# Optimization experiments

Measured on AMD Instinct MI355X. Metric: run time of the kernel, lower is better.

Reference implementation:

```python
import jax, jax.numpy as jnp
import numpy as np

# nuScenes-scale config: batch 2, 360x360 BEV grid (1440/4), 128 channels,
# 10 classes, 200 proposals, 3x3 NMS kernel, 40k occupied voxels per sample.
B, H, W_GRID, NUM_CLS, NUM_PROP, NMS_K = 2, 360, 360, 10, 200, 3
C = 128
N_PER_B = 40000
NEG_FILL = -1000000.0  # scatter_nd fill value from to_dense()


def _bev_pos():
    # replicates create_2D_grid: coord = (x_index_along_dim1, y_index_along_dim0)
    xs = jnp.arange(H, dtype=jnp.float32)
    ys = jnp.arange(W_GRID, dtype=jnp.float32)
    by, bx = jnp.meshgrid(xs, ys, indexing='ij')  # by[i,j]=i, bx[i,j]=j
    return jnp.stack([bx, by], axis=-1).reshape(-1, 2)  # [H*W, 2]


def setup_inputs() -> dict:
    key = jax.random.key(0)
    ks = jax.random.split(key, 10)
    # unique spatial locations per batch sample (sparse voxel coords)
    flats = [jax.random.permutation(ks[i], H * W_GRID)[:N_PER_B] for i in range(B)]
    flat = jnp.concatenate(flats)
    b = jnp.repeat(jnp.arange(B), N_PER_B)
    indices = jnp.stack([b, flat // W_GRID, flat % W_GRID], axis=1).astype(jnp.int32)
    features = jax.random.normal(ks[4], (B * N_PER_B, C), jnp.float32)
    # heatmap head (pointwise linears standing in for the submconv stack)
    W_hm1 = jax.random.normal(ks[5], (C, C), jnp.float32) * (2.0 / C) ** 0.5
    b_hm1 = jnp.zeros((C,), jnp.float32)
    W_hm2 = jax.random.normal(ks[6], (C, NUM_CLS), jnp.float32) * (2.0 / C) ** 0.5
    b_hm2 = jnp.full((NUM_CLS,), -2.19, jnp.float32)  # fc[-1].bias.fill_(-2.19)
    # class_encoding: nn.Conv1d(num_class, channels, 1)
    W_cls = jax.random.normal(ks[7], (C, NUM_CLS), jnp.float32) * 0.1
    b_cls = jnp.zeros((C,), jnp.float32)
    return dict(features=features, W_hm1=W_hm1, b_hm1=b_hm1, W_hm2=W_hm2,
                b_hm2=b_hm2, W_cls=W_cls, b_cls=b_cls, indices=indices)


def reference(features, W_hm1, b_hm1, W_hm2, b_hm2, W_cls, b_cls, indices):
    bidx, yi, xi = indices[:, 0], indices[:, 1], indices[:, 2]
    HW = H * W_GRID

    # --- x.dense(): scatter voxel features to dense BEV grid (zero fill) ---
    xd = jnp.zeros((B, H, W_GRID, C), features.dtype).at[bidx, yi, xi].set(features)
    x_flat = xd.reshape(B, HW, C).transpose(0, 2, 1)  # [B, C, HW]

    # --- heatmap head (per-voxel) then to_dense() with -1e6 fill ---
    hm = jax.nn.relu(features @ W_hm1 + b_hm1) @ W_hm2 + b_hm2  # [N, NUM_CLS]
    dense_hm = jnp.full((B, H, W_GRID, NUM_CLS), NEG_FILL, hm.dtype)
    dense_hm = dense_hm.at[bidx, yi, xi].set(hm).transpose(0, 3, 1, 2)  # [B,K,H,W]

    heat = jax.nn.sigmoid(dense_hm)  # detached in original

    # --- NMS-kernel peak extraction ---
    pad = NMS_K // 2
    inner = jax.lax.reduce_window(heat, -jnp.inf, jax.lax.max,
                                  (1, 1, NMS_K, NMS_K), (1, 1, 1, 1), 'VALID')
    local_max = jnp.zeros_like(heat).at[:, :, pad:H - pad, pad:W_GRID - pad].set(inner)
    # pedestrian (8) and traffic_cone (9): kernel size 1
    local_max = local_max.at[:, 8].set(heat[:, 8]).at[:, 9].set(heat[:, 9])
    heat = heat * (heat == local_max)
    heat_f = heat.reshape(B, NUM_CLS, HW)

    # --- top-k proposals over (class, location) ---
    _, top = jax.lax.top_k(heat_f.reshape(B, -1), NUM_PROP)  # [B, P]
    cls = top // HW
    idx = top % HW

    # --- gather proposal features + class encoding ---
    qf = jnp.take_along_axis(x_flat, jnp.broadcast_to(idx[:, None, :], (B, C, NUM_PROP)), axis=2)
    onehot = jax.nn.one_hot(cls, NUM_CLS, dtype=qf.dtype)  # [B, P, K]
    qf = qf + jnp.einsum('ck,bpk->bcp', W_cls, onehot) + b_cls[None, :, None]

    # --- proposal positions and heatmap scores ---
    query_pos = _bev_pos()[idx]  # [B, P, 2]
    qhs = jnp.take_along_axis(heat_f, jnp.broadcast_to(idx[:, None, :], (B, NUM_CLS, NUM_PROP)), axis=2)
    return qf, query_pos, qhs, cls
```

## Files before the change

kernel.cpp:

```cpp
#include <hip/hip_runtime.h>

#define HW 129600
#define WG 360
#define HG 360
#define NCLS 10
#define NPROP 200
#define CDIM 128
#define NROWS 80000
#define NB 2
#define SEL_CAP 4096
#define HIST_BINS 16384
#define CHUNK 8192

__device__ __forceinline__ float nms_val(const float* __restrict__ hp, int pos,
                                         int cl) {
  float v = hp[pos];
  if (cl >= 8) return v;
  int y = pos / WG, x = pos - y * WG;
  if (y == 0 || y == HG - 1 || x == 0 || x == WG - 1) return 0.f;
  float m = v;
  m = fmaxf(m, hp[pos - 1]);
  m = fmaxf(m, hp[pos + 1]);
  m = fmaxf(m, hp[pos - WG - 1]);
  m = fmaxf(m, hp[pos - WG]);
  m = fmaxf(m, hp[pos - WG + 1]);
  m = fmaxf(m, hp[pos + WG - 1]);
  m = fmaxf(m, hp[pos + WG]);
  m = fmaxf(m, hp[pos + WG + 1]);
  return (v == m) ? v : 0.f;
}

__global__ __launch_bounds__(128) void k_head(
    const float* __restrict__ feat, const float* __restrict__ W1,
    const float* __restrict__ b1, const float* __restrict__ W2,
    const float* __restrict__ b2, const int* __restrict__ idxs,
    float* __restrict__ dense_heat, int* __restrict__ rowmap) {
  __shared__ __align__(16) float lds_w[32 * 128];
  __shared__ __align__(16) float lds_f[32 * 32];
  __shared__ __align__(16) float lds_w2t[NCLS * 128];
  __shared__ int lds_b[32];
  __shared__ int lds_p[32];
  const int tid = threadIdx.x;
  const int row0 = blockIdx.x * 32;
  const int tc = tid & 31;
  const int tr = tid >> 5;

  float acc[8][4];
#pragma unroll
  for (int r = 0; r < 8; ++r) {
#pragma unroll
    for (int c = 0; c < 4; ++c) acc[r][c] = 0.f;
  }

  for (int kt = 0; kt < 4; ++kt) {
#pragma unroll
    for (int i = 0; i < 8; ++i) {
      int fi = tid + i * 128;
      *(float4*)(lds_w + fi * 4) = *(const float4*)(W1 + kt * 4096 + fi * 4);
    }
#pragma unroll
    for (int i = 0; i < 2; ++i) {
      int fi = tid + i * 128;
      int r = fi >> 3, kq = fi & 7;
      *(float4*)(lds_f + r * 32 + kq * 4) =
          *(const float4*)(feat + (size_t)(row0 + r) * CDIM + kt * 32 + kq * 4);
    }
    __syncthreads();
#pragma unroll
    for (int kg = 0; kg < 8; ++kg) {
      float4 w0 = *(const float4*)(lds_w + (kg * 4 + 0) * 128 + tc * 4);
      float4 w1 = *(const float4*)(lds_w + (kg * 4 + 1) * 128 + tc * 4);
      float4 w2 = *(const float4*)(lds_w + (kg * 4 + 2) * 128 + tc * 4);
      float4 w3 = *(const float4*)(lds_w + (kg * 4 + 3) * 128 + tc * 4);
#pragma unroll
      for (int r = 0; r < 8; ++r) {
        float4 fv = *(const float4*)(lds_f + (tr * 8 + r) * 32 + kg * 4);
        acc[r][0] = fmaf(fv.x, w0.x, acc[r][0]);
        acc[r][0] = fmaf(fv.y, w1.x, acc[r][0]);
        acc[r][0] = fmaf(fv.z, w2.x, acc[r][0]);
        acc[r][0] = fmaf(fv.w, w3.x, acc[r][0]);
        acc[r][1] = fmaf(fv.x, w0.y, acc[r][1]);
        acc[r][1] = fmaf(fv.y, w1.y, acc[r][1]);
        acc[r][1] = fmaf(fv.z, w2.y, acc[r][1]);
        acc[r][1] = fmaf(fv.w, w3.y, acc[r][1]);
        acc[r][2] = fmaf(fv.x, w0.z, acc[r][2]);
        acc[r][2] = fmaf(fv.y, w1.z, acc[r][2]);
        acc[r][2] = fmaf(fv.z, w2.z, acc[r][2]);
        acc[r][2] = fmaf(fv.w, w3.z, acc[r][2]);
        acc[r][3] = fmaf(fv.x, w0.w, acc[r][3]);
        acc[r][3] = fmaf(fv.y, w1.w, acc[r][3]);
        acc[r][3] = fmaf(fv.z, w2.w, acc[r][3]);
        acc[r][3] = fmaf(fv.w, w3.w, acc[r][3]);
      }
    }
    __syncthreads();
  }

  float4 b1v = *(const float4*)(b1 + tc * 4);
#pragma unroll
  for (int r = 0; r < 8; ++r) {
    float4 h;
    h.x = fmaxf(acc[r][0] + b1v.x, 0.f);
    h.y = fmaxf(acc[r][1] + b1v.y, 0.f);
    h.z = fmaxf(acc[r][2] + b1v.z, 0.f);
    h.w = fmaxf(acc[r][3] + b1v.w, 0.f);
    *(float4*)(lds_w + (tr * 8 + r) * 128 + tc * 4) = h;
  }
  for (int i = tid; i < CDIM * NCLS; i += 128) {
    int k = i / NCLS, j = i - k * NCLS;
    lds_w2t[j * 128 + k] = W2[i];
  }
  if (tid < 32) {
    int row = row0 + tid;
    int bb = idxs[row * 3 + 0];
    int yy = idxs[row * 3 + 1];
    int xx = idxs[row * 3 + 2];
    lds_b[tid] = bb;
    lds_p[tid] = yy * WG + xx;
    rowmap[(size_t)bb * HW + yy * WG + xx] = row;
  }
  __syncthreads();

#pragma unroll
  for (int oo = 0; oo < 3; ++oo) {
    int o = tid + oo * 128;
    if (o < 32 * NCLS) {
      int r = o / NCLS, j = o - r * NCLS;
      float s = b2[j];
      for (int i4 = 0; i4 < 32; ++i4) {
        int k4 = (i4 + tid) & 31;
        float4 hv = *(const float4*)(lds_w + r * 128 + k4 * 4);
        float4 wv = *(const float4*)(lds_w2t + j * 128 + k4 * 4);
        s = fmaf(hv.x, wv.x, s);
        s = fmaf(hv.y, wv.y, s);
        s = fmaf(hv.z, wv.z, s);
        s = fmaf(hv.w, wv.w, s);
      }
      float heat = 1.0f / (1.0f + expf(-s));
      dense_heat[((size_t)lds_b[r] * NCLS + j) * HW + lds_p[r]] = heat;
    }
  }
}

__global__ __launch_bounds__(256) void k_nms_hist(
    const float* __restrict__ dense_heat, unsigned int* __restrict__ hist) {
  __shared__ unsigned int lh[HIST_BINS];
  const int cl = blockIdx.y;
  const int b = blockIdx.z;
  const int p0 = blockIdx.x * CHUNK;
  for (int i = threadIdx.x; i < HIST_BINS; i += 256) lh[i] = 0;
  __syncthreads();
  const float* hp = dense_heat + ((size_t)b * NCLS + cl) * HW;
  for (int it = 0; it < CHUNK; it += 256) {
    int pos = p0 + it + threadIdx.x;
    if (pos < HW) {
      float out = nms_val(hp, pos, cl);
      if (out > 0.f) atomicAdd(&lh[__float_as_uint(out) >> 16], 1u);
    }
  }
  __syncthreads();
  unsigned int* gh = hist + (size_t)b * HIST_BINS;
  for (int i = threadIdx.x; i < HIST_BINS; i += 256) {
    unsigned int c = lh[i];
    if (c) atomicAdd(&gh[i], c);
  }
}

__global__ __launch_bounds__(256) void k_thresh(
    const unsigned int* __restrict__ hist, int* __restrict__ selT) {
  __shared__ unsigned int coarse[256];
  const int b = blockIdx.x;
  const unsigned int* h = hist + (size_t)b * HIST_BINS;
  unsigned int s = 0;
  for (int i = 0; i < 64; ++i) s += h[threadIdx.x * 64 + i];
  coarse[threadIdx.x] = s;
  __syncthreads();
  if (threadIdx.x == 0) {
    unsigned int cum = 0;
    int T = 0;
    int ci = 255;
    for (; ci >= 0; --ci) {
      if (cum + coarse[ci] >= NPROP) break;
      cum += coarse[ci];
    }
    if (ci >= 0) {
      int t = 63;
      for (; t > 0; --t) {
        unsigned int c = h[ci * 64 + t];
        if (cum + c >= NPROP) break;
        cum += c;
      }
      T = ci * 64 + t;
    }
    selT[b] = T;
  }
}

__global__ __launch_bounds__(256) void k_collect(
    const float* __restrict__ dense_heat, const int* __restrict__ selT,
    unsigned long long* __restrict__ sel, int* __restrict__ sel_cnt) {
  const int cl = blockIdx.y;
  const int b = blockIdx.z;
  const int pos = blockIdx.x * 256 + threadIdx.x;
  float out = 0.f;
  if (pos < HW)
    out = nms_val(dense_heat + ((size_t)b * NCLS + cl) * HW, pos, cl);
  unsigned int bits = __float_as_uint(out);
  bool pred = (out > 0.f) && ((int)(bits >> 16) >= selT[b]);
  unsigned long long mask = __ballot(pred);
  if (pred) {
    int lane = threadIdx.x & 63;
    int lb = __popcll(mask & ((1ull << lane) - 1ull));
    int base = 0;
    if (lb == 0) base = atomicAdd(&sel_cnt[b], (int)__popcll(mask));
    base = __builtin_amdgcn_readfirstlane(base);
    unsigned int gidx = (unsigned int)cl * HW + (unsigned int)pos;
    unsigned long long key =
        ((unsigned long long)bits << 32) | (unsigned long long)(~gidx);
    int slot = base + lb;
    if (slot < SEL_CAP) sel[(size_t)b * SEL_CAP + slot] = key;
  }
}

__global__ __launch_bounds__(256) void k_final(
    const unsigned long long* __restrict__ sel, const int* __restrict__ sel_cnt,
    const float* __restrict__ dense_heat, const int* __restrict__ rowmap,
    const float* __restrict__ feat, const float* __restrict__ Wc,
    const float* __restrict__ bc, float* __restrict__ out) {
  __shared__ unsigned long long sk[SEL_CAP];
  const int b = blockIdx.x;
  const int tid = threadIdx.x;
  int M = sel_cnt[b];
  if (M > SEL_CAP) M = SEL_CAP;
  int n = 256;
  while (n < M) n <<= 1;
  for (int i = tid; i < n; i += 256)
    sk[i] = (i < M) ? sel[(size_t)b * SEL_CAP + i] : 0ull;
  __syncthreads();
  for (int k = 2; k <= n; k <<= 1) {
    for (int j = k >> 1; j > 0; j >>= 1) {
      for (int t = tid; t < n; t += 256) {
        int l = t ^ j;
        if (l > t) {
          unsigned long long a = sk[t], c = sk[l];
          bool up = ((t & k) == 0);
          if (up ? (a < c) : (a > c)) {
            sk[t] = c;
            sk[l] = a;
          }
        }
      }
      __syncthreads();
    }
  }
  if (tid < NPROP) {
    const int p = tid;
    unsigned long long key = sk[p];
    unsigned int bits = (unsigned int)(key >> 32);
    unsigned int gidx = ~((unsigned int)(key & 0xFFFFFFFFull));
    if (bits == 0u) gidx = 0u;
    int cls = (int)(gidx / HW);
    int pos = (int)(gidx - (unsigned int)cls * HW);
    int y = pos / WG, x = pos - y * WG;
    out[51200 + ((size_t)b * NPROP + p) * 2 + 0] = (float)x;
    out[51200 + ((size_t)b * NPROP + p) * 2 + 1] = (float)y;
    out[56000 + b * NPROP + p] = (float)cls;
    for (int k = 0; k < NCLS; ++k) {
      const float* hp = dense_heat + ((size_t)b * NCLS + k) * HW;
      out[52000 + ((size_t)b * NCLS + k) * NPROP + p] = nms_val(hp, pos, k);
    }
    int row = rowmap[(size_t)b * HW + pos];
    if (bits == 0u) row = 0;
    const float* fr = feat + (size_t)row * CDIM;
    for (int c = 0; c < CDIM; ++c) {
      out[((size_t)b * CDIM + c) * NPROP + p] = fr[c] + Wc[c * NCLS + cls] + bc[c];
    }
  }
}

extern "C" void kernel_launch(void* const* d_in, const int* in_sizes, int n_in,
                              void* d_out, int out_size, void* d_ws,
                              size_t ws_size, hipStream_t stream) {
  const float* feat = (const float*)d_in[0];
  const float* W1 = (const float*)d_in[1];
  const float* b1 = (const float*)d_in[2];
  const float* W2 = (const float*)d_in[3];
  const float* b2 = (const float*)d_in[4];
  const float* Wc = (const float*)d_in[5];
  const float* bc = (const float*)d_in[6];
  const int* idxs = (const int*)d_in[7];
  float* out = (float*)d_out;

  char* ws = (char*)d_ws;
  float* dense_heat = (float*)(ws + 0);
  unsigned int* hist = (unsigned int*)(ws + 10368000);
  int* rowmap = (int*)(ws + 10499072);
  unsigned long long* sel = (unsigned long long*)(ws + 11535872);
  int* cnts = (int*)(ws + 11601408);
  int* sel_cnt = cnts + 0;
  int* selT = cnts + 2;

  hipMemsetAsync(dense_heat, 0, (size_t)NB * NCLS * HW * sizeof(float), stream);
  hipMemsetAsync(hist, 0, (size_t)NB * HIST_BINS * sizeof(unsigned int), stream);
  hipMemsetAsync(cnts, 0, 4 * sizeof(int), stream);

  k_head<<<NROWS / 32, 128, 0, stream>>>(feat, W1, b1, W2, b2, idxs, dense_heat,
                                         rowmap);
  k_nms_hist<<<dim3((HW + CHUNK - 1) / CHUNK, NCLS, NB), 256, 0, stream>>>(
      dense_heat, hist);
  k_thresh<<<NB, 256, 0, stream>>>(hist, selT);
  k_collect<<<dim3((HW + 255) / 256, NCLS, NB), 256, 0, stream>>>(
      dense_heat, selT, sel, sel_cnt);
  k_final<<<NB, 256, 0, stream>>>(sel, sel_cnt, dense_heat, rowmap, feat, Wc, bc,
                                  out);
}
```

Baseline: 204.4 us.

## Rework head GEMM, fuse threshold into collect, rank-select top-k, coalesce final writes

The MLP head now keeps a 64-row feature tile in padded LDS. Each wavefront computes 32 output channels per row, reading W1 through wave-uniform scalar loads, and the 10-class projection is reduced across the four waves through LDS. The threshold kernel is folded into the collect kernel, where every block recomputes the threshold from a coarser 4096-bin histogram, removing one launch. The bitonic sort in the final kernel is replaced by an O(M^2) rank count, and the output writes are rearranged so consecutive threads write consecutive addresses. The coarser histogram can let more candidates through (capacity raised to 8192), which makes the quadratic ranking costlier. Having every collect block redo the threshold scan adds redundant work.

Result: slower. 209.5 us (+2.5%).

```diff
diff --git a/kernel.cpp b/kernel.cpp
--- a/kernel.cpp
+++ b/kernel.cpp
@@ -8,9 +8,11 @@
 #define CDIM 128
 #define NROWS 80000
 #define NB 2
-#define SEL_CAP 4096
-#define HIST_BINS 16384
-#define CHUNK 8192
+#define SEL_CAP 8192
+#define HBINS 4096
+#define CHUNK 4096
+#define RPB 64
+#define FSTRIDE 132
 
 __device__ __forceinline__ float nms_val(const float* __restrict__ hp, int pos,
                                          int cl) {
@@ -30,87 +32,18 @@
   return (v == m) ? v : 0.f;
 }
 
-__global__ __launch_bounds__(128) void k_head(
+__global__ __launch_bounds__(256) void k_head(
     const float* __restrict__ feat, const float* __restrict__ W1,
     const float* __restrict__ b1, const float* __restrict__ W2,
     const float* __restrict__ b2, const int* __restrict__ idxs,
     float* __restrict__ dense_heat, int* __restrict__ rowmap) {
-  __shared__ __align__(16) float lds_w[32 * 128];
-  __shared__ __align__(16) float lds_f[32 * 32];
-  __shared__ __align__(16) float lds_w2t[NCLS * 128];
-  __shared__ int lds_b[32];
-  __shared__ int lds_p[32];
+  __shared__ __align__(16) float lds_f[RPB * FSTRIDE];
+  __shared__ int lds_b[RPB];
+  __shared__ int lds_p[RPB];
   const int tid = threadIdx.x;
-  const int row0 = blockIdx.x * 32;
-  const int tc = tid & 31;
-  const int tr = tid >> 5;
-
-  float acc[8][4];
-#pragma unroll
-  for (int r = 0; r < 8; ++r) {
-#pragma unroll
-    for (int c = 0; c < 4; ++c) acc[r][c] = 0.f;
-  }
-
-  for (int kt = 0; kt < 4; ++kt) {
-#pragma unroll
-    for (int i = 0; i < 8; ++i) {
-      int fi = tid + i * 128;
-      *(float4*)(lds_w + fi * 4) = *(const float4*)(W1 + kt * 4096 + fi * 4);
-    }
-#pragma unroll
-    for (int i = 0; i < 2; ++i) {
-      int fi = tid + i * 128;
-      int r = fi >> 3, kq = fi & 7;
-      *(float4*)(lds_f + r * 32 + kq * 4) =
-          *(const float4*)(feat + (size_t)(row0 + r) * CDIM + kt * 32 + kq * 4);
-    }
-    __syncthreads();
-#pragma unroll
-    for (int kg = 0; kg < 8; ++kg) {
-      float4 w0 = *(const float4*)(lds_w + (kg * 4 + 0) * 128 + tc * 4);
-      float4 w1 = *(const float4*)(lds_w + (kg * 4 + 1) * 128 + tc * 4);
-      float4 w2 = *(const float4*)(lds_w + (kg * 4 + 2) * 128 + tc * 4);
-      float4 w3 = *(const float4*)(lds_w + (kg * 4 + 3) * 128 + tc * 4);
-#pragma unroll
-      for (int r = 0; r < 8; ++r) {
-        float4 fv = *(const float4*)(lds_f + (tr * 8 + r) * 32 + kg * 4);
-        acc[r][0] = fmaf(fv.x, w0.x, acc[r][0]);
-        acc[r][0] = fmaf(fv.y, w1.x, acc[r][0]);
-        acc[r][0] = fmaf(fv.z, w2.x, acc[r][0]);
-        acc[r][0] = fmaf(fv.w, w3.x, acc[r][0]);
-        acc[r][1] = fmaf(fv.x, w0.y, acc[r][1]);
-        acc[r][1] = fmaf(fv.y, w1.y, acc[r][1]);
-        acc[r][1] = fmaf(fv.z, w2.y, acc[r][1]);
-        acc[r][1] = fmaf(fv.w, w3.y, acc[r][1]);
-        acc[r][2] = fmaf(fv.x, w0.z, acc[r][2]);
-        acc[r][2] = fmaf(fv.y, w1.z, acc[r][2]);
-        acc[r][2] = fmaf(fv.z, w2.z, acc[r][2]);
-        acc[r][2] = fmaf(fv.w, w3.z, acc[r][2]);
-        acc[r][3] = fmaf(fv.x, w0.w, acc[r][3]);
-        acc[r][3] = fmaf(fv.y, w1.w, acc[r][3]);
-        acc[r][3] = fmaf(fv.z, w2.w, acc[r][3]);
-        acc[r][3] = fmaf(fv.w, w3.w, acc[r][3]);
-      }
-    }
-    __syncthreads();
-  }
-
-  float4 b1v = *(const float4*)(b1 + tc * 4);
-#pragma unroll
-  for (int r = 0; r < 8; ++r) {
-    float4 h;
-    h.x = fmaxf(acc[r][0] + b1v.x, 0.f);
-    h.y = fmaxf(acc[r][1] + b1v.y, 0.f);
-    h.z = fmaxf(acc[r][2] + b1v.z, 0.f);
-    h.w = fmaxf(acc[r][3] + b1v.w, 0.f);
-    *(float4*)(lds_w + (tr * 8 + r) * 128 + tc * 4) = h;
-  }
-  for (int i = tid; i < CDIM * NCLS; i += 128) {
-    int k = i / NCLS, j = i - k * NCLS;
-    lds_w2t[j * 128 + k] = W2[i];
-  }
-  if (tid < 32) {
+  const int row0 = blockIdx.x * RPB;
+
+  if (tid < RPB) {
     int row = row0 + tid;
     int bb = idxs[row * 3 + 0];
     int yy = idxs[row * 3 + 1];
@@ -119,60 +52,100 @@
     lds_p[tid] = yy * WG + xx;
     rowmap[(size_t)bb * HW + yy * WG + xx] = row;
   }
-  __syncthreads();
-
-#pragma unroll
-  for (int oo = 0; oo < 3; ++oo) {
-    int o = tid + oo * 128;
-    if (o < 32 * NCLS) {
-      int r = o / NCLS, j = o - r * NCLS;
-      float s = b2[j];
-      for (int i4 = 0; i4 < 32; ++i4) {
-        int k4 = (i4 + tid) & 31;
-        float4 hv = *(const float4*)(lds_w + r * 128 + k4 * 4);
-        float4 wv = *(const float4*)(lds_w2t + j * 128 + k4 * 4);
-        s = fmaf(hv.x, wv.x, s);
-        s = fmaf(hv.y, wv.y, s);
-        s = fmaf(hv.z, wv.z, s);
-        s = fmaf(hv.w, wv.w, s);
+#pragma unroll
+  for (int i = 0; i < 8; ++i) {
+    int fi = tid + i * 256;
+    int r = fi >> 5, k4 = fi & 31;
+    float4 v = *(const float4*)(feat + (size_t)(row0 + r) * CDIM + k4 * 4);
+    *(float4*)(lds_f + r * FSTRIDE + k4 * 4) = v;
+  }
+  __syncthreads();
+
+  const int lane = tid & 63;
+  const int c0 = __builtin_amdgcn_readfirstlane((tid >> 6) << 5);
+  float acc[32];
+#pragma unroll
+  for (int c = 0; c < 32; ++c) acc[c] = 0.f;
+
+  const float* fr = lds_f + lane * FSTRIDE;
+  for (int k = 0; k < CDIM; k += 4) {
+    float4 f4 = *(const float4*)(fr + k);
+#pragma unroll
+    for (int h = 0; h < 2; ++h) {
+#pragma unroll
+      for (int cc = 0; cc < 16; ++cc) {
+        const int c = c0 + h * 16 + cc;
+        float a = acc[h * 16 + cc];
+        a = fmaf(f4.x, W1[(k + 0) * CDIM + c], a);
+        a = fmaf(f4.y, W1[(k + 1) * CDIM + c], a);
+        a = fmaf(f4.z, W1[(k + 2) * CDIM + c], a);
+        a = fmaf(f4.w, W1[(k + 3) * CDIM + c], a);
+        acc[h * 16 + cc] = a;
       }
-      float heat = 1.0f / (1.0f + expf(-s));
-      dense_heat[((size_t)lds_b[r] * NCLS + j) * HW + lds_p[r]] = heat;
-    }
+    }
+  }
+
+  float p[NCLS];
+#pragma unroll
+  for (int j = 0; j < NCLS; ++j) p[j] = 0.f;
+#pragma unroll
+  for (int cc = 0; cc < 32; ++cc) {
+    const int c = c0 + cc;
+    float hv = fmaxf(acc[cc] + b1[c], 0.f);
+#pragma unroll
+    for (int j = 0; j < NCLS; ++j) p[j] = fmaf(hv, W2[c * NCLS + j], p[j]);
+  }
+
+  __syncthreads();
+  float* part = lds_f;
+  {
+    const int w = tid >> 6;
+#pragma unroll
+    for (int j = 0; j < NCLS; ++j) part[w * (RPB * NCLS) + lane * NCLS + j] = p[j];
+  }
+  __syncthreads();
+  for (int o = tid; o < RPB * NCLS; o += 256) {
+    int r = o / NCLS, j = o - r * NCLS;
+    float s = part[o] + part[640 + o] + part[1280 + o] + part[1920 + o] + b2[j];
+    float heat = 1.0f / (1.0f + expf(-s));
+    dense_heat[((size_t)lds_b[r] * NCLS + j) * HW + lds_p[r]] = heat;
   }
 }
 
 __global__ __launch_bounds__(256) void k_nms_hist(
     const float* __restrict__ dense_heat, unsigned int* __restrict__ hist) {
-  __shared__ unsigned int lh[HIST_BINS];
+  __shared__ unsigned int lh[HBINS];
   const int cl = blockIdx.y;
   const int b = blockIdx.z;
   const int p0 = blockIdx.x * CHUNK;
-  for (int i = threadIdx.x; i < HIST_BINS; i += 256) lh[i] = 0;
+  for (int i = threadIdx.x; i < HBINS; i += 256) lh[i] = 0;
   __syncthreads();
   const float* hp = dense_heat + ((size_t)b * NCLS + cl) * HW;
   for (int it = 0; it < CHUNK; it += 256) {
     int pos = p0 + it + threadIdx.x;
     if (pos < HW) {
       float out = nms_val(hp, pos, cl);
-      if (out > 0.f) atomicAdd(&lh[__float_as_uint(out) >> 16], 1u);
-    }
-  }
-  __syncthreads();
-  unsigned int* gh = hist + (size_t)b * HIST_BINS;
-  for (int i = threadIdx.x; i < HIST_BINS; i += 256) {
+      if (out > 0.f) atomicAdd(&lh[__float_as_uint(out) >> 18], 1u);
+    }
+  }
+  __syncthreads();
+  unsigned int* gh = hist + (size_t)b * HBINS;
+  for (int i = threadIdx.x; i < HBINS; i += 256) {
     unsigned int c = lh[i];
     if (c) atomicAdd(&gh[i], c);
   }
 }
 
-__global__ __launch_bounds__(256) void k_thresh(
-    const unsigned int* __restrict__ hist, int* __restrict__ selT) {
+__global__ __launch_bounds__(256) void k_collect(
+    const float* __restrict__ dense_heat, const unsigned int* __restrict__ hist,
+    unsigned long long* __restrict__ sel, int* __restrict__ sel_cnt) {
   __shared__ unsigned int coarse[256];
-  const int b = blockIdx.x;
-  const unsigned int* h = hist + (size_t)b * HIST_BINS;
+  __shared__ int sT;
+  const int cl = blockIdx.y;
+  const int b = blockIdx.z;
+  const unsigned int* h = hist + (size_t)b * HBINS;
   unsigned int s = 0;
-  for (int i = 0; i < 64; ++i) s += h[threadIdx.x * 64 + i];
+  for (int i = 0; i < 16; ++i) s += h[threadIdx.x * 16 + i];
   coarse[threadIdx.x] = s;
   __syncthreads();
   if (threadIdx.x == 0) {
@@ -184,41 +157,39 @@
       cum += coarse[ci];
     }
     if (ci >= 0) {
-      int t = 63;
+      int t = 15;
       for (; t > 0; --t) {
-        unsigned int c = h[ci * 64 + t];
+        unsigned int c = h[ci * 16 + t];
         if (cum + c >= NPROP) break;
         cum += c;
       }
-      T = ci * 64 + t;
-    }
-    selT[b] = T;
-  }
-}
-
-__global__ __launch_bounds__(256) void k_collect(
-    const float* __restrict__ dense_heat, const int* __restrict__ selT,
-    unsigned long long* __restrict__ sel, int* __restrict__ sel_cnt) {
-  const int cl = blockIdx.y;
-  const int b = blockIdx.z;
-  const int pos = blockIdx.x * 256 + threadIdx.x;
-  float out = 0.f;
-  if (pos < HW)
-    out = nms_val(dense_heat + ((size_t)b * NCLS + cl) * HW, pos, cl);
-  unsigned int bits = __float_as_uint(out);
-  bool pred = (out > 0.f) && ((int)(bits >> 16) >= selT[b]);
-  unsigned long long mask = __ballot(pred);
-  if (pred) {
-    int lane = threadIdx.x & 63;
-    int lb = __popcll(mask & ((1ull << lane) - 1ull));
-    int base = 0;
-    if (lb == 0) base = atomicAdd(&sel_cnt[b], (int)__popcll(mask));
-    base = __builtin_amdgcn_readfirstlane(base);
-    unsigned int gidx = (unsigned int)cl * HW + (unsigned int)pos;
-    unsigned long long key =
-        ((unsigned long long)bits << 32) | (unsigned long long)(~gidx);
-    int slot = base + lb;
-    if (slot < SEL_CAP) sel[(size_t)b * SEL_CAP + slot] = key;
+      T = ci * 16 + t;
+    }
+    sT = T;
+  }
+  __syncthreads();
+  const int T = sT;
+  const float* hp = dense_heat + ((size_t)b * NCLS + cl) * HW;
+  const int p0 = blockIdx.x * CHUNK;
+  for (int it = 0; it < CHUNK; it += 256) {
+    int pos = p0 + it + threadIdx.x;
+    float out = 0.f;
+    if (pos < HW) out = nms_val(hp, pos, cl);
+    unsigned int bits = __float_as_uint(out);
+    bool pred = (out > 0.f) && ((int)(bits >> 18) >= T);
+    unsigned long long mask = __ballot(pred);
+    if (pred) {
+      int lane = threadIdx.x & 63;
+      int lb = __popcll(mask & ((1ull << lane) - 1ull));
+      int base = 0;
+      if (lb == 0) base = atomicAdd(&sel_cnt[b], (int)__popcll(mask));
+      base = __builtin_amdgcn_readfirstlane(base);
+      unsigned int gidx = (unsigned int)cl * HW + (unsigned int)pos;
+      unsigned long long key =
+          ((unsigned long long)bits << 32) | (unsigned long long)(~gidx);
+      int slot = base + lb;
+      if (slot < SEL_CAP) sel[(size_t)b * SEL_CAP + slot] = key;
+    }
   }
 }
 
@@ -228,53 +199,46 @@
     const float* __restrict__ feat, const float* __restrict__ Wc,
     const float* __restrict__ bc, float* __restrict__ out) {
   __shared__ unsigned long long sk[SEL_CAP];
+  __shared__ unsigned long long winners[NPROP];
+  __shared__ int wpos[NPROP];
+  __shared__ int wcls[NPROP];
+  __shared__ int wrow[NPROP];
   const int b = blockIdx.x;
   const int tid = threadIdx.x;
   int M = sel_cnt[b];
   if (M > SEL_CAP) M = SEL_CAP;
-  int n = 256;
-  while (n < M) n <<= 1;
-  for (int i = tid; i < n; i += 256)
-    sk[i] = (i < M) ? sel[(size_t)b * SEL_CAP + i] : 0ull;
-  __syncthreads();
-  for (int k = 2; k <= n; k <<= 1) {
-    for (int j = k >> 1; j > 0; j >>= 1) {
-      for (int t = tid; t < n; t += 256) {
-        int l = t ^ j;
-        if (l > t) {
-          unsigned long long a = sk[t], c = sk[l];
-          bool up = ((t & k) == 0);
-          if (up ? (a < c) : (a > c)) {
-            sk[t] = c;
-            sk[l] = a;
-          }
-        }
-      }
-      __syncthreads();
-    }
-  }
+  for (int i = tid; i < M; i += 256) sk[i] = sel[(size_t)b * SEL_CAP + i];
+  __syncthreads();
+  for (int i = tid; i < M; i += 256) {
+    unsigned long long key = sk[i];
+    int rank = 0;
+    for (int j = 0; j < M; ++j) rank += (sk[j] > key) ? 1 : 0;
+    if (rank < NPROP) winners[rank] = key;
+  }
+  __syncthreads();
   if (tid < NPROP) {
-    const int p = tid;
-    unsigned long long key = sk[p];
-    unsigned int bits = (unsigned int)(key >> 32);
+    unsigned long long key = winners[tid];
     unsigned int gidx = ~((unsigned int)(key & 0xFFFFFFFFull));
-    if (bits == 0u) gidx = 0u;
     int cls = (int)(gidx / HW);
     int pos = (int)(gidx - (unsigned int)cls * HW);
     int y = pos / WG, x = pos - y * WG;
-    out[51200 + ((size_t)b * NPROP + p) * 2 + 0] = (float)x;
-    out[51200 + ((size_t)b * NPROP + p) * 2 + 1] = (float)y;
-    out[56000 + b * NPROP + p] = (float)cls;
-    for (int k = 0; k < NCLS; ++k) {
-      const float* hp = dense_heat + ((size_t)b * NCLS + k) * HW;
-      out[52000 + ((size_t)b * NCLS + k) * NPROP + p] = nms_val(hp, pos, k);
-    }
-    int row = rowmap[(size_t)b * HW + pos];
-    if (bits == 0u) row = 0;
-    const float* fr = feat + (size_t)row * CDIM;
-    for (int c = 0; c < CDIM; ++c) {
-      out[((size_t)b * CDIM + c) * NPROP + p] = fr[c] + Wc[c * NCLS + cls] + bc[c];
-    }
+    wpos[tid] = pos;
+    wcls[tid] = cls;
+    wrow[tid] = rowmap[(size_t)b * HW + pos];
+    out[51200 + ((size_t)b * NPROP + tid) * 2 + 0] = (float)x;
+    out[51200 + ((size_t)b * NPROP + tid) * 2 + 1] = (float)y;
+    out[56000 + b * NPROP + tid] = (float)cls;
+  }
+  __syncthreads();
+  for (int o = tid; o < NCLS * NPROP; o += 256) {
+    int j = o / NPROP, pp = o - j * NPROP;
+    const float* hp = dense_heat + ((size_t)b * NCLS + j) * HW;
+    out[52000 + (size_t)b * NCLS * NPROP + o] = nms_val(hp, wpos[pp], j);
+  }
+  for (int o = tid; o < CDIM * NPROP; o += 256) {
+    int c = o / NPROP, pp = o - c * NPROP;
+    out[(size_t)b * CDIM * NPROP + o] =
+        feat[(size_t)wrow[pp] * CDIM + c] + Wc[c * NCLS + wcls[pp]] + bc[c];
   }
 }
 
@@ -294,23 +258,20 @@
   char* ws = (char*)d_ws;
   float* dense_heat = (float*)(ws + 0);
   unsigned int* hist = (unsigned int*)(ws + 10368000);
-  int* rowmap = (int*)(ws + 10499072);
-  unsigned long long* sel = (unsigned long long*)(ws + 11535872);
-  int* cnts = (int*)(ws + 11601408);
-  int* sel_cnt = cnts + 0;
-  int* selT = cnts + 2;
+  int* rowmap = (int*)(ws + 10400768);
+  unsigned long long* sel = (unsigned long long*)(ws + 11437568);
+  int* sel_cnt = (int*)(ws + 11568640);
 
   hipMemsetAsync(dense_heat, 0, (size_t)NB * NCLS * HW * sizeof(float), stream);
-  hipMemsetAsync(hist, 0, (size_t)NB * HIST_BINS * sizeof(unsigned int), stream);
-  hipMemsetAsync(cnts, 0, 4 * sizeof(int), stream);
-
-  k_head<<<NROWS / 32, 128, 0, stream>>>(feat, W1, b1, W2, b2, idxs, dense_heat,
-                                         rowmap);
+  hipMemsetAsync(hist, 0, (size_t)NB * HBINS * sizeof(unsigned int), stream);
+  hipMemsetAsync(sel_cnt, 0, 2 * sizeof(int), stream);
+
+  k_head<<<NROWS / RPB, 256, 0, stream>>>(feat, W1, b1, W2, b2, idxs, dense_heat,
+                                          rowmap);
   k_nms_hist<<<dim3((HW + CHUNK - 1) / CHUNK, NCLS, NB), 256, 0, stream>>>(
       dense_heat, hist);
-  k_thresh<<<NB, 256, 0, stream>>>(hist, selT);
-  k_collect<<<dim3((HW + 255) / 256, NCLS, NB), 256, 0, stream>>>(
-      dense_heat, selT, sel, sel_cnt);
+  k_collect<<<dim3((HW + CHUNK - 1) / CHUNK, NCLS, NB), 256, 0, stream>>>(
+      dense_heat, hist, sel, sel_cnt);
   k_final<<<NB, 256, 0, stream>>>(sel, sel_cnt, dense_heat, rowmap, feat, Wc, bc,
                                   out);
 }
```
